# Performance work log

Hardware: AMD Instinct MI355X
Metric: run time of the kernel (lower is better)

The kernel has to match this reference:

```python
import jax, jax.numpy as jnp
import numpy as np

TOP_K = 2
NOISE_STDDEV = 1.0


def setup_inputs() -> dict:
    key = jax.random.key(0)
    k1, k2, k3, k4 = jax.random.split(key, 4)
    N, D, E = 16384, 2048, 64
    x = jax.random.normal(k1, (N, D), dtype=jnp.float32)
    W_gate = jax.random.normal(k2, (E, D), dtype=jnp.float32) * (1.0 / np.sqrt(D))
    W_noise = jax.random.normal(k3, (E, D), dtype=jnp.float32) * (1.0 / np.sqrt(D))
    noise = jax.random.normal(k4, (N, E), dtype=jnp.float32)
    return {"x": x, "W_gate": W_gate, "W_noise": W_noise, "noise": noise}


def reference(x, W_gate, W_noise, noise):
    # clean gating logits: [N, E]
    clean_logits = jnp.einsum("nd,ed->ne", x, W_gate)
    # noise scale via softplus of second projection (training mode)
    noise_scale = jax.nn.softplus(jnp.einsum("nd,ed->ne", x, W_noise))
    noisy_logits = clean_logits + noise_scale * noise * NOISE_STDDEV
    # top-k selection then softmax over the k selected logits
    top_k_logits, top_k_indices = jax.lax.top_k(noisy_logits, TOP_K)
    combined_weights = jax.nn.softmax(top_k_logits, axis=-1)
    return (combined_weights, top_k_indices, clean_logits)
```

## Files before the change

### kernel.cpp

```cpp
#include <hip/hip_runtime.h>
#include <math.h>


constexpr int NROWS = 16384;
constexpr int DDIM  = 2048;
constexpr int EDIM  = 64;
constexpr int BM    = 128;
constexpr int NKS   = 32;
constexpr int IDX_OFF   = NROWS * 2;
constexpr int CLEAN_OFF = NROWS * 4;
constexpr size_t WPACK = 262144;
constexpr int XS    = 16384;
constexpr int NBUF  = 4;

typedef _Float16 f16x8 __attribute__((ext_vector_type(8)));
typedef float    f32x4 __attribute__((ext_vector_type(4)));

__device__ __forceinline__ float softplus_f(float z) {
    return fmaxf(z, 0.0f) + log1pf(expf(-fabsf(z)));
}

__device__ __forceinline__ void gload16(const void* g, void* l) {
    __builtin_amdgcn_global_load_lds(
        (const __attribute__((address_space(1))) unsigned int*)g,
        (__attribute__((address_space(3))) unsigned int*)l, 16, 0, 0);
}

__global__ __launch_bounds__(256) void split_w_kernel(
    const float* __restrict__ Wg, const float* __restrict__ Wn,
    _Float16* __restrict__ wh, _Float16* __restrict__ wl)
{
    const int t    = blockIdx.x * 256 + threadIdx.x;
    const int grp  = t >> 6;
    const int lane = t & 63;
    const int kc   = grp >> 3;
    const int cg   = (grp >> 1) & 3;
    const int cf   = grp & 1;
    const int col  = cg * 32 + cf * 16 + (lane & 15);
    const int k0   = kc * 32 + (lane >> 4) * 8;
    const float* src = (col < 64) ? &Wg[(size_t)col * DDIM + k0]
                                  : &Wn[(size_t)(col - 64) * DDIM + k0];
    const float4 v0 = *reinterpret_cast<const float4*>(src);
    const float4 v1 = *reinterpret_cast<const float4*>(src + 4);
    float vv[8] = {v0.x, v0.y, v0.z, v0.w, v1.x, v1.y, v1.z, v1.w};
    union { _Float16 h[8]; uint4 u; } hh, ll;
    #pragma unroll
    for (int j = 0; j < 8; ++j) {
        hh.h[j] = (_Float16)vv[j];
        ll.h[j] = (_Float16)((vv[j] - (float)hh.h[j]) * 2048.0f);
    }
    const size_t off = (size_t)grp * 512 + lane * 8;
    *reinterpret_cast<uint4*>(&wh[off]) = hh.u;
    *reinterpret_cast<uint4*>(&wl[off]) = ll.u;
}

__device__ __forceinline__ void split8(const float4 a, const float4 b, f16x8& h, f16x8& l) {
    const float v[8] = {a.x, a.y, a.z, a.w, b.x, b.y, b.z, b.w};
    #pragma unroll
    for (int j = 0; j < 8; ++j) {
        const _Float16 hh = (_Float16)v[j];
        h[j] = hh;
        l[j] = (_Float16)((v[j] - (float)hh) * 2048.0f);
    }
}

__global__ __launch_bounds__(1024, 4) void gemm_part_kernel(
    const float* __restrict__ x,
    const _Float16* __restrict__ whp,
    const _Float16* __restrict__ wlp,
    float* __restrict__ pbuf)
{
    extern __shared__ __align__(16) unsigned char smem[];

    const int tid  = threadIdx.x;
    const int lane = tid & 63;
    const int wid  = tid >> 6;
    const int rg   = wid >> 2;
    const int cg   = wid & 3;
    const int g    = (lane >> 4) & 3;
    const int idx  = lane & 15;
    const int kh   = blockIdx.x >> 7;
    const int rt   = blockIdx.x & 127;
    const int row_base = rt * BM;

    const int sr  = tid >> 3;
    const int sq  = tid & 7;
    const int sq2 = sq ^ (sr & 7);
    const float* xsrc = x + (size_t)(row_base + sr) * DDIM + kh * 1024 + sq2 * 4;

    const char* bh2 = (const char*)whp + (size_t)kh * 262144 + (cg * 2) * 1024 + lane * 16;
    const char* bl2 = (const char*)wlp + (size_t)kh * 262144 + (cg * 2) * 1024 + lane * 16;

    int aoff[2][2];
    #pragma unroll
    for (int rf = 0; rf < 2; ++rf) {
        const int row = rg * 32 + rf * 16 + idx;
        #pragma unroll
        for (int j = 0; j < 2; ++j)
            aoff[rf][j] = row * 128 + (((2 * g + j) ^ (row & 7)) << 4);
    }

    f32x4 accm[2][2], accc[2][2];
    #pragma unroll
    for (int rf = 0; rf < 2; ++rf)
        #pragma unroll
        for (int cf = 0; cf < 2; ++cf) { accm[rf][cf] = (f32x4)0.0f; accc[rf][cf] = (f32x4)0.0f; }

    auto stageX = [&](int u) {
        gload16(xsrc + u * 32, smem + (u & (NBUF - 1)) * XS + tid * 16);
    };
    auto loadW = [&](int u, float4& h0, float4& h1, float4& l0, float4& l1) {
        const char* ph = bh2 + (size_t)u * 8192;
        const char* pl = bl2 + (size_t)u * 8192;
        h0 = *reinterpret_cast<const float4*>(ph);
        h1 = *reinterpret_cast<const float4*>(ph + 1024);
        l0 = *reinterpret_cast<const float4*>(pl);
        l1 = *reinterpret_cast<const float4*>(pl + 1024);
    };

    auto compute = [&](int t, const float4& h0, const float4& h1,
                       const float4& l0, const float4& l1) {
        const int b = (t & (NBUF - 1)) * XS;
        const float4 a00 = *reinterpret_cast<const float4*>(&smem[b + aoff[0][0]]);
        const float4 a01 = *reinterpret_cast<const float4*>(&smem[b + aoff[0][1]]);
        const float4 a10 = *reinterpret_cast<const float4*>(&smem[b + aoff[1][0]]);
        const float4 a11 = *reinterpret_cast<const float4*>(&smem[b + aoff[1][1]]);
        const f16x8 Bh0 = __builtin_bit_cast(f16x8, h0);
        const f16x8 Bh1 = __builtin_bit_cast(f16x8, h1);
        const f16x8 Bl0 = __builtin_bit_cast(f16x8, l0);
        const f16x8 Bl1 = __builtin_bit_cast(f16x8, l1);

        f16x8 Ah0, Al0, Ah1, Al1;
        split8(a00, a01, Ah0, Al0);
        split8(a10, a11, Ah1, Al1);

        accm[0][0] = __builtin_amdgcn_mfma_f32_16x16x32_f16(Ah0, Bh0, accm[0][0], 0, 0, 0);
        accm[0][1] = __builtin_amdgcn_mfma_f32_16x16x32_f16(Ah0, Bh1, accm[0][1], 0, 0, 0);
        accm[1][0] = __builtin_amdgcn_mfma_f32_16x16x32_f16(Ah1, Bh0, accm[1][0], 0, 0, 0);
        accm[1][1] = __builtin_amdgcn_mfma_f32_16x16x32_f16(Ah1, Bh1, accm[1][1], 0, 0, 0);
        accc[0][0] = __builtin_amdgcn_mfma_f32_16x16x32_f16(Al0, Bh0, accc[0][0], 0, 0, 0);
        accc[0][1] = __builtin_amdgcn_mfma_f32_16x16x32_f16(Al0, Bh1, accc[0][1], 0, 0, 0);
        accc[1][0] = __builtin_amdgcn_mfma_f32_16x16x32_f16(Al1, Bh0, accc[1][0], 0, 0, 0);
        accc[1][1] = __builtin_amdgcn_mfma_f32_16x16x32_f16(Al1, Bh1, accc[1][1], 0, 0, 0);
        accc[0][0] = __builtin_amdgcn_mfma_f32_16x16x32_f16(Ah0, Bl0, accc[0][0], 0, 0, 0);
        accc[0][1] = __builtin_amdgcn_mfma_f32_16x16x32_f16(Ah0, Bl1, accc[0][1], 0, 0, 0);
        accc[1][0] = __builtin_amdgcn_mfma_f32_16x16x32_f16(Ah1, Bl0, accc[1][0], 0, 0, 0);
        accc[1][1] = __builtin_amdgcn_mfma_f32_16x16x32_f16(Ah1, Bl1, accc[1][1], 0, 0, 0);
    };

    float4 s0h0, s0h1, s0l0, s0l1, s1h0, s1h1, s1l0, s1l1;

    stageX(0); loadW(0, s0h0, s0h1, s0l0, s0l1);
    stageX(1); loadW(1, s1h0, s1h1, s1l0, s1l1);
    __builtin_amdgcn_sched_barrier(0);

    for (int tt = 0; tt < 15; ++tt) {
        const int t0 = 2 * tt;
        stageX(t0 + 2);
        asm volatile("s_waitcnt vmcnt(6)" ::: "memory");
        __builtin_amdgcn_s_barrier();
        __builtin_amdgcn_sched_barrier(0);
        compute(t0, s0h0, s0h1, s0l0, s0l1);
        loadW(t0 + 2, s0h0, s0h1, s0l0, s0l1);
        __builtin_amdgcn_sched_barrier(0);
        stageX(t0 + 3);
        asm volatile("s_waitcnt vmcnt(6)" ::: "memory");
        __builtin_amdgcn_s_barrier();
        __builtin_amdgcn_sched_barrier(0);
        compute(t0 + 1, s1h0, s1h1, s1l0, s1l1);
        loadW(t0 + 3, s1h0, s1h1, s1l0, s1l1);
        __builtin_amdgcn_sched_barrier(0);
    }
    asm volatile("s_waitcnt vmcnt(5)" ::: "memory");
    __builtin_amdgcn_s_barrier();
    __builtin_amdgcn_sched_barrier(0);
    compute(30, s0h0, s0h1, s0l0, s0l1);
    asm volatile("s_waitcnt vmcnt(0)" ::: "memory");
    __builtin_amdgcn_s_barrier();
    __builtin_amdgcn_sched_barrier(0);
    compute(31, s1h0, s1h1, s1l0, s1l1);

    float* dst = pbuf + (size_t)kh * NROWS * 128;
    #pragma unroll
    for (int rf = 0; rf < 2; ++rf)
        #pragma unroll
        for (int cf = 0; cf < 2; ++cf) {
            const int col = cg * 32 + cf * 16 + idx;
            #pragma unroll
            for (int q = 0; q < 4; ++q) {
                const int lrow = rg * 32 + rf * 16 + g * 4 + q;
                dst[(size_t)(row_base + lrow) * 128 + col] =
                    accm[rf][cf][q] + accc[rf][cf][q] * 4.8828125e-4f;
            }
        }
}

__global__ __launch_bounds__(256) void reduce_topk_kernel(
    const float* __restrict__ pbuf,
    const float* __restrict__ noise,
    float* __restrict__ out)
{
    const int tid = threadIdx.x;
    const int row = tid >> 3;
    const int j   = tid & 7;
    const int e0  = j * 8;
    const int grow = blockIdx.x * 32 + row;

    const float* p0 = pbuf + (size_t)grow * 128;
    const float* p1 = pbuf + (size_t)(NROWS + grow) * 128;

    float4 c0 = *reinterpret_cast<const float4*>(&p0[e0]);
    float4 c1 = *reinterpret_cast<const float4*>(&p0[e0 + 4]);
    float4 s0 = *reinterpret_cast<const float4*>(&p0[64 + e0]);
    float4 s1 = *reinterpret_cast<const float4*>(&p0[64 + e0 + 4]);
    const float4 d0 = *reinterpret_cast<const float4*>(&p1[e0]);
    const float4 d1 = *reinterpret_cast<const float4*>(&p1[e0 + 4]);
    const float4 t0 = *reinterpret_cast<const float4*>(&p1[64 + e0]);
    const float4 t1 = *reinterpret_cast<const float4*>(&p1[64 + e0 + 4]);
    c0.x += d0.x; c0.y += d0.y; c0.z += d0.z; c0.w += d0.w;
    c1.x += d1.x; c1.y += d1.y; c1.z += d1.z; c1.w += d1.w;
    s0.x += t0.x; s0.y += t0.y; s0.z += t0.z; s0.w += t0.w;
    s1.x += t1.x; s1.y += t1.y; s1.z += t1.z; s1.w += t1.w;

    *reinterpret_cast<float4*>(&out[CLEAN_OFF + (size_t)grow * EDIM + e0])     = c0;
    *reinterpret_cast<float4*>(&out[CLEAN_OFF + (size_t)grow * EDIM + e0 + 4]) = c1;

    const float4 z0 = *reinterpret_cast<const float4*>(&noise[(size_t)grow * EDIM + e0]);
    const float4 z1 = *reinterpret_cast<const float4*>(&noise[(size_t)grow * EDIM + e0 + 4]);

    float nv[8];
    nv[0] = fmaf(softplus_f(s0.x), z0.x, c0.x);
    nv[1] = fmaf(softplus_f(s0.y), z0.y, c0.y);
    nv[2] = fmaf(softplus_f(s0.z), z0.z, c0.z);
    nv[3] = fmaf(softplus_f(s0.w), z0.w, c0.w);
    nv[4] = fmaf(softplus_f(s1.x), z1.x, c1.x);
    nv[5] = fmaf(softplus_f(s1.y), z1.y, c1.y);
    nv[6] = fmaf(softplus_f(s1.z), z1.z, c1.z);
    nv[7] = fmaf(softplus_f(s1.w), z1.w, c1.w);

    float v0 = nv[0], v1 = -INFINITY;
    int   i0 = e0,    i1 = -1;
    #pragma unroll
    for (int m = 1; m < 8; ++m) {
        const float v = nv[m]; const int e = e0 + m;
        if (v > v0)      { v1 = v0; i1 = i0; v0 = v; i0 = e; }
        else if (v > v1) { v1 = v;  i1 = e; }
    }
    #pragma unroll
    for (int d = 1; d < 8; d <<= 1) {
        const float ov0 = __shfl_xor(v0, d); const int oi0 = __shfl_xor(i0, d);
        const float ov1 = __shfl_xor(v1, d); const int oi1 = __shfl_xor(i1, d);
        const bool aFirst = (v0 > ov0) || (v0 == ov0 && i0 < oi0);
        float n0, n1; int ni0, ni1;
        if (aFirst) {
            n0 = v0; ni0 = i0;
            const bool s = (v1 > ov0) || (v1 == ov0 && i1 < oi0);
            n1 = s ? v1 : ov0; ni1 = s ? i1 : oi0;
        } else {
            n0 = ov0; ni0 = oi0;
            const bool s = (ov1 > v0) || (ov1 == v0 && oi1 < i0);
            n1 = s ? ov1 : v0; ni1 = s ? oi1 : i0;
        }
        v0 = n0; i0 = ni0; v1 = n1; i1 = ni1;
    }
    if (j == 0) {
        const float ex = expf(v1 - v0);
        const float w0 = 1.0f / (1.0f + ex);
        const float w1 = 1.0f - w0;
        out[(size_t)grow * 2 + 0] = w0;
        out[(size_t)grow * 2 + 1] = w1;
        out[IDX_OFF + (size_t)grow * 2 + 0] = (float)i0;
        out[IDX_OFF + (size_t)grow * 2 + 1] = (float)i1;
    }
}

extern "C" void kernel_launch(void* const* d_in, const int* in_sizes, int n_in,
                              void* d_out, int out_size, void* d_ws, size_t ws_size,
                              hipStream_t stream) {
    const float* x     = (const float*)d_in[0];
    const float* Wg    = (const float*)d_in[1];
    const float* Wn    = (const float*)d_in[2];
    const float* noise = (const float*)d_in[3];
    float* out = (float*)d_out;

    _Float16* wh = (_Float16*)d_ws;
    _Float16* wl = wh + WPACK;
    float* pbuf  = (float*)((char*)d_ws + (1 << 20));

    split_w_kernel<<<dim3(128), dim3(256), 0, stream>>>(Wg, Wn, wh, wl);
    gemm_part_kernel<<<dim3(256), dim3(1024), NBUF * XS, stream>>>(x, wh, wl, pbuf);
    reduce_topk_kernel<<<dim3(NROWS / 32), dim3(256), 0, stream>>>(pbuf, noise, out);
}
```

Baseline: 51.17 us.

## Give each wave a private double-buffered LDS tile to drop block barriers

Each of the 16 waves now stages its own 32-row slice of x into a private 8 KB double-buffered LDS region instead of sharing a 4-deep block-wide buffer. That removes every s_barrier from the K loop, so waves sync only through their own vmcnt and lgkmcnt waits. In exchange, the four column-group waves sharing a row group each load the same x rows, quadrupling global and L2 traffic for x. LDS use also rises to 128 KB per block, which limits occupancy to one block per CU.

```diff
diff --git a/kernel.cpp b/kernel.cpp
--- a/kernel.cpp
+++ b/kernel.cpp
@@ -10,8 +10,7 @@
 constexpr int IDX_OFF   = NROWS * 2;
 constexpr int CLEAN_OFF = NROWS * 4;
 constexpr size_t WPACK = 262144;
-constexpr int XS    = 16384;
-constexpr int NBUF  = 4;
+constexpr int LDSSZ = 131072;
 
 typedef _Float16 f16x8 __attribute__((ext_vector_type(8)));
 typedef float    f32x4 __attribute__((ext_vector_type(4)));
@@ -82,11 +81,14 @@
     const int kh   = blockIdx.x >> 7;
     const int rt   = blockIdx.x & 127;
     const int row_base = rt * BM;
-
-    const int sr  = tid >> 3;
-    const int sq  = tid & 7;
-    const int sq2 = sq ^ (sr & 7);
-    const float* xsrc = x + (size_t)(row_base + sr) * DDIM + kh * 1024 + sq2 * 4;
+    const int wpriv = wid * 8192;
+
+    const int lrow = lane >> 3;
+    const int sq2  = (lane & 7) ^ lrow;
+    const float* xp[4];
+    #pragma unroll
+    for (int i = 0; i < 4; ++i)
+        xp[i] = x + (size_t)(row_base + rg * 32 + i * 8 + lrow) * DDIM + kh * 1024 + sq2 * 4;
 
     const char* bh2 = (const char*)whp + (size_t)kh * 262144 + (cg * 2) * 1024 + lane * 16;
     const char* bl2 = (const char*)wlp + (size_t)kh * 262144 + (cg * 2) * 1024 + lane * 16;
@@ -94,10 +96,10 @@
     int aoff[2][2];
     #pragma unroll
     for (int rf = 0; rf < 2; ++rf) {
-        const int row = rg * 32 + rf * 16 + idx;
+        const int r = rf * 16 + idx;
         #pragma unroll
         for (int j = 0; j < 2; ++j)
-            aoff[rf][j] = row * 128 + (((2 * g + j) ^ (row & 7)) << 4);
+            aoff[rf][j] = r * 128 + (((2 * g + j) ^ (r & 7)) << 4);
     }
 
     f32x4 accm[2][2], accc[2][2];
@@ -106,8 +108,11 @@
         #pragma unroll
         for (int cf = 0; cf < 2; ++cf) { accm[rf][cf] = (f32x4)0.0f; accc[rf][cf] = (f32x4)0.0f; }
 
-    auto stageX = [&](int u) {
-        gload16(xsrc + u * 32, smem + (u & (NBUF - 1)) * XS + tid * 16);
+    auto stageA = [&](int u) {
+        unsigned char* db = smem + wpriv + (u & 1) * 4096;
+        #pragma unroll
+        for (int i = 0; i < 4; ++i)
+            gload16(xp[i] + u * 32, db + i * 1024 + lane * 16);
     };
     auto loadW = [&](int u, float4& h0, float4& h1, float4& l0, float4& l1) {
         const char* ph = bh2 + (size_t)u * 8192;
@@ -118,22 +123,17 @@
         l1 = *reinterpret_cast<const float4*>(pl + 1024);
     };
 
-    auto compute = [&](int t, const float4& h0, const float4& h1,
-                       const float4& l0, const float4& l1) {
-        const int b = (t & (NBUF - 1)) * XS;
-        const float4 a00 = *reinterpret_cast<const float4*>(&smem[b + aoff[0][0]]);
-        const float4 a01 = *reinterpret_cast<const float4*>(&smem[b + aoff[0][1]]);
-        const float4 a10 = *reinterpret_cast<const float4*>(&smem[b + aoff[1][0]]);
-        const float4 a11 = *reinterpret_cast<const float4*>(&smem[b + aoff[1][1]]);
+    auto mfma12 = [&](const float4& a00, const float4& a01,
+                      const float4& a10, const float4& a11,
+                      const float4& h0, const float4& h1,
+                      const float4& l0, const float4& l1) {
         const f16x8 Bh0 = __builtin_bit_cast(f16x8, h0);
         const f16x8 Bh1 = __builtin_bit_cast(f16x8, h1);
         const f16x8 Bl0 = __builtin_bit_cast(f16x8, l0);
         const f16x8 Bl1 = __builtin_bit_cast(f16x8, l1);
-
         f16x8 Ah0, Al0, Ah1, Al1;
         split8(a00, a01, Ah0, Al0);
         split8(a10, a11, Ah1, Al1);
-
         accm[0][0] = __builtin_amdgcn_mfma_f32_16x16x32_f16(Ah0, Bh0, accm[0][0], 0, 0, 0);
         accm[0][1] = __builtin_amdgcn_mfma_f32_16x16x32_f16(Ah0, Bh1, accm[0][1], 0, 0, 0);
         accm[1][0] = __builtin_amdgcn_mfma_f32_16x16x32_f16(Ah1, Bh0, accm[1][0], 0, 0, 0);
@@ -148,37 +148,47 @@
         accc[1][1] = __builtin_amdgcn_mfma_f32_16x16x32_f16(Ah1, Bl1, accc[1][1], 0, 0, 0);
     };
 
+    #define BODY(T, H0, H1, L0, L1, STAGE)                                         \
+    {                                                                              \
+        asm volatile("s_waitcnt vmcnt(8)" ::: "memory");                           \
+        __builtin_amdgcn_sched_barrier(0);                                         \
+        const unsigned char* rb = smem + wpriv + ((T) & 1) * 4096;                 \
+        const float4 a00 = *reinterpret_cast<const float4*>(rb + aoff[0][0]);      \
+        const float4 a01 = *reinterpret_cast<const float4*>(rb + aoff[0][1]);      \
+        const float4 a10 = *reinterpret_cast<const float4*>(rb + aoff[1][0]);      \
+        const float4 a11 = *reinterpret_cast<const float4*>(rb + aoff[1][1]);      \
+        asm volatile("s_waitcnt lgkmcnt(0)" ::: "memory");                         \
+        __builtin_amdgcn_sched_barrier(0);                                         \
+        if (STAGE) stageA((T) + 2);                                                \
+        mfma12(a00, a01, a10, a11, H0, H1, L0, L1);                                \
+        if (STAGE) loadW((T) + 2, H0, H1, L0, L1);                                 \
+        __builtin_amdgcn_sched_barrier(0);                                         \
+    }
+
     float4 s0h0, s0h1, s0l0, s0l1, s1h0, s1h1, s1l0, s1l1;
 
-    stageX(0); loadW(0, s0h0, s0h1, s0l0, s0l1);
-    stageX(1); loadW(1, s1h0, s1h1, s1l0, s1l1);
+    stageA(0); loadW(0, s0h0, s0h1, s0l0, s0l1);
+    stageA(1); loadW(1, s1h0, s1h1, s1l0, s1l1);
     __builtin_amdgcn_sched_barrier(0);
 
     for (int tt = 0; tt < 15; ++tt) {
-        const int t0 = 2 * tt;
-        stageX(t0 + 2);
-        asm volatile("s_waitcnt vmcnt(6)" ::: "memory");
-        __builtin_amdgcn_s_barrier();
+        BODY(2 * tt,     s0h0, s0h1, s0l0, s0l1, 1);
+        BODY(2 * tt + 1, s1h0, s1h1, s1l0, s1l1, 1);
+    }
+    BODY(30, s0h0, s0h1, s0l0, s0l1, 0);
+    {
+        asm volatile("s_waitcnt vmcnt(0)" ::: "memory");
         __builtin_amdgcn_sched_barrier(0);
-        compute(t0, s0h0, s0h1, s0l0, s0l1);
-        loadW(t0 + 2, s0h0, s0h1, s0l0, s0l1);
+        const unsigned char* rb = smem + wpriv + (31 & 1) * 4096;
+        const float4 a00 = *reinterpret_cast<const float4*>(rb + aoff[0][0]);
+        const float4 a01 = *reinterpret_cast<const float4*>(rb + aoff[0][1]);
+        const float4 a10 = *reinterpret_cast<const float4*>(rb + aoff[1][0]);
+        const float4 a11 = *reinterpret_cast<const float4*>(rb + aoff[1][1]);
+        asm volatile("s_waitcnt lgkmcnt(0)" ::: "memory");
         __builtin_amdgcn_sched_barrier(0);
-        stageX(t0 + 3);
-        asm volatile("s_waitcnt vmcnt(6)" ::: "memory");
-        __builtin_amdgcn_s_barrier();
-        __builtin_amdgcn_sched_barrier(0);
-        compute(t0 + 1, s1h0, s1h1, s1l0, s1l1);
-        loadW(t0 + 3, s1h0, s1h1, s1l0, s1l1);
-        __builtin_amdgcn_sched_barrier(0);
-    }
-    asm volatile("s_waitcnt vmcnt(5)" ::: "memory");
-    __builtin_amdgcn_s_barrier();
-    __builtin_amdgcn_sched_barrier(0);
-    compute(30, s0h0, s0h1, s0l0, s0l1);
-    asm volatile("s_waitcnt vmcnt(0)" ::: "memory");
-    __builtin_amdgcn_s_barrier();
-    __builtin_amdgcn_sched_barrier(0);
-    compute(31, s1h0, s1h1, s1l0, s1l1);
+        mfma12(a00, a01, a10, a11, s1h0, s1h1, s1l0, s1l1);
+    }
+    #undef BODY
 
     float* dst = pbuf + (size_t)kh * NROWS * 128;
     #pragma unroll
@@ -188,8 +198,8 @@
             const int col = cg * 32 + cf * 16 + idx;
             #pragma unroll
             for (int q = 0; q < 4; ++q) {
-                const int lrow = rg * 32 + rf * 16 + g * 4 + q;
-                dst[(size_t)(row_base + lrow) * 128 + col] =
+                const int lrow2 = rg * 32 + rf * 16 + g * 4 + q;
+                dst[(size_t)(row_base + lrow2) * 128 + col] =
                     accm[rf][cf][q] + accc[rf][cf][q] * 4.8828125e-4f;
             }
         }
@@ -288,6 +298,6 @@
     float* pbuf  = (float*)((char*)d_ws + (1 << 20));
 
     split_w_kernel<<<dim3(128), dim3(256), 0, stream>>>(Wg, Wn, wh, wl);
-    gemm_part_kernel<<<dim3(256), dim3(1024), NBUF * XS, stream>>>(x, wh, wl, pbuf);
+    gemm_part_kernel<<<dim3(256), dim3(1024), LDSSZ, stream>>>(x, wh, wl, pbuf);
     reduce_topk_kernel<<<dim3(NROWS / 32), dim3(256), 0, stream>>>(pbuf, noise, out);
 }
```

Result: slower. 63.89 us (+24.8%).
